# Kernel tuning notes

Hardware: AMD Instinct MI355X
Metric: run time of the kernel (lower is better)

Reference implementation:

```python
import jax, jax.numpy as jnp
import numpy as np


def setup_inputs() -> dict:
    key = jax.random.key(0)
    k1, k2, k3, k4, k5 = jax.random.split(key, 5)
    B, S, E, T = 64, 2048, 256, 100
    h = jax.random.normal(k1, (B, S, E), dtype=jnp.float32)
    theta = jax.random.uniform(k2, (B, T), dtype=jnp.float32)
    w = jax.random.normal(k3, (E, T), dtype=jnp.float32) * 0.05
    v = jax.random.normal(k4, (E, 1), dtype=jnp.float32) * 0.05
    u = jax.random.normal(k5, (E, E), dtype=jnp.float32) * 0.05
    return {"h": h, "theta": theta, "w": w, "v": v, "u": u}


def reference(h, theta, w, v, u):
    # h: [B,S,E], theta: [B,T], w: [E,T], v: [E,1], u: [E,E]
    theta_w = theta @ w.T                      # [B,E]
    h_u = jnp.einsum('bse,ef->bsf', h, u)      # [B,S,E]
    g = jnp.tanh(theta_w[:, None, :] + h_u) @ v  # [B,S,1]
    weight = jax.nn.softmax(g[..., 0], axis=-1)  # [B,S]
    vec = jnp.einsum('bs,bse->be', weight, h)    # [B,E]
    return vec
```

## Files before the change

kernel.cpp:

```cpp
#include <hip/hip_runtime.h>
#include <hip/hip_bf16.h>
#include <math.h>


#define E_DIM 256
#define GM 32
#define NC 8

typedef __bf16 bf16x8 __attribute__((ext_vector_type(8)));
typedef float  f32x4  __attribute__((ext_vector_type(4)));

__device__ __forceinline__ unsigned short f2bf(float x) {
    return __builtin_bit_cast(unsigned short, (__bf16)x);
}

__device__ __forceinline__ float fast_tanh(float x) {
    const float e = __expf(2.0f * x);
    const float r = __builtin_amdgcn_rcpf(e + 1.0f);
    return fmaf(-2.0f, r, 1.0f);
}

__device__ __forceinline__ unsigned sswz(unsigned slot, unsigned row) {
    return (slot & 48u) | ((slot & 15u) ^ (row & 15u));
}

__global__ __launch_bounds__(256) void k_prep(const float* __restrict__ u,
                                              const float* __restrict__ theta,
                                              const float* __restrict__ w,
                                              unsigned short* __restrict__ u_t,
                                              float* __restrict__ tw,
                                              int T) {
    if (blockIdx.x < 16) {
        __shared__ float tl[256 * 17];
        const int f0 = blockIdx.x * 16;
        const int tid = threadIdx.x;
        const int cl = tid & 15;
        const int rw = tid >> 4;
#pragma unroll
        for (int it = 0; it < 16; ++it) {
            const int e = it * 16 + rw;
            tl[e * 17 + cl] = u[(size_t)e * E_DIM + f0 + cl];
        }
        __syncthreads();
        unsigned short outv[16];
#pragma unroll
        for (int j = 0; j < 16; ++j)
            outv[j] = f2bf(tl[(cl * 16 + j) * 17 + rw]);
        *reinterpret_cast<uint4*>(u_t + (size_t)(f0 + rw) * E_DIM + cl * 16) =
            *reinterpret_cast<const uint4*>(outv);
        *reinterpret_cast<uint4*>(u_t + (size_t)(f0 + rw) * E_DIM + cl * 16 + 8) =
            *reinterpret_cast<const uint4*>(outv + 8);
    } else {
        __shared__ float th[128];
        const int b = blockIdx.x - 16;
        const int e = threadIdx.x;
        if (threadIdx.x < T) th[threadIdx.x] = theta[b * T + threadIdx.x];
        __syncthreads();
        float acc = 0.f;
        for (int t = 0; t < T; ++t) acc = fmaf(th[t], w[e * T + t], acc);
        tw[b * E_DIM + e] = acc;
    }
}

__global__
__attribute__((amdgpu_flat_work_group_size(256, 256), amdgpu_waves_per_eu(2, 2)))
void k_fused(const float* __restrict__ h,
             const unsigned short* __restrict__ u_t,
             const float* __restrict__ tw_,
             const float* __restrict__ v,
             float* __restrict__ partial,
             float* __restrict__ pd,
             int S, int SC) {
    __shared__ float Abuf[2][GM * E_DIM];
    __shared__ float red[4][GM];
    __shared__ float pacc[4][E_DIM];
    __shared__ float dred[4];

    const int b   = blockIdx.y;
    const int c0  = blockIdx.x * NC;
    const int tid = threadIdx.x;
    const int w   = tid >> 6;
    const int l   = tid & 63;
    const int lg  = l >> 4;
    const int lc  = l & 15;
    const int f0w = w * 64;

#define STAGE(buf, ch)                                                           \
    {                                                                            \
        const char* hb_ = (const char*)(h + ((size_t)b * S + (size_t)(ch) * GM) * E_DIM); \
        _Pragma("unroll")                                                        \
        for (int r = 0; r < 8; ++r) {                                            \
            const int row = r * 4 + w;                                           \
            const unsigned ss = sswz((unsigned)l, (unsigned)row);                \
            __builtin_amdgcn_global_load_lds(                                    \
                (const __attribute__((address_space(1))) void*)(hb_ + (size_t)row * 1024 + ss * 16), \
                (__attribute__((address_space(3))) void*)((char*)Abuf[buf] + r * 4096 + w * 1024), \
                16, 0, 0);                                                       \
        }                                                                        \
    }

    STAGE(0, c0);

    bf16x8 ub[8][4];
#pragma unroll
    for (int kt = 0; kt < 8; ++kt)
#pragma unroll
        for (int n = 0; n < 4; ++n)
            ub[kt][n] = *reinterpret_cast<const bf16x8*>(
                u_t + (size_t)(f0w + n * 16 + lc) * E_DIM + kt * 32 + lg * 8);

    float tw_f[4], v_f[4];
#pragma unroll
    for (int n = 0; n < 4; ++n) {
        const int f = f0w + n * 16 + lc;
        tw_f[n] = tw_[b * E_DIM + f];
        v_f[n]  = v[f];
    }

    f32x4 numa = (f32x4){0.f, 0.f, 0.f, 0.f};
    float den = 0.f;

    for (int c = 0; c < NC; ++c) {
        const int cur = c & 1;

        if (c + 1 < NC) {
            STAGE(cur ^ 1, c0 + c + 1);
            asm volatile("s_waitcnt vmcnt(8)" ::: "memory");
        } else {
            asm volatile("s_waitcnt vmcnt(0)" ::: "memory");
        }
        __builtin_amdgcn_s_barrier();
        __builtin_amdgcn_sched_barrier(0);

        const char* A = (const char*)Abuf[cur];
        f32x4 acc[2][4];
#pragma unroll
        for (int m = 0; m < 2; ++m)
#pragma unroll
            for (int n = 0; n < 4; ++n)
                acc[m][n] = (f32x4){0.f, 0.f, 0.f, 0.f};

#pragma unroll
        for (int kt = 0; kt < 8; ++kt) {
            bf16x8 af[2];
#pragma unroll
            for (int m = 0; m < 2; ++m) {
                const unsigned row = (unsigned)(m * 16 + lc);
                const unsigned s0 = sswz((unsigned)(kt * 8 + lg * 2), row);
                const unsigned s1 = sswz((unsigned)(kt * 8 + lg * 2 + 1), row);
                const f32x4 fa0 = *reinterpret_cast<const f32x4*>(A + row * 1024 + s0 * 16);
                const f32x4 fa1 = *reinterpret_cast<const f32x4*>(A + row * 1024 + s1 * 16);
#pragma unroll
                for (int j = 0; j < 4; ++j) {
                    af[m][j]     = (__bf16)fa0[j];
                    af[m][4 + j] = (__bf16)fa1[j];
                }
            }
#pragma unroll
            for (int n = 0; n < 4; ++n) {
                acc[0][n] = __builtin_amdgcn_mfma_f32_16x16x32_bf16(af[0], ub[kt][n], acc[0][n], 0, 0, 0);
                acc[1][n] = __builtin_amdgcn_mfma_f32_16x16x32_bf16(af[1], ub[kt][n], acc[1][n], 0, 0, 0);
            }
        }

        float rs[2][4] = {};
#pragma unroll
        for (int n = 0; n < 4; ++n)
#pragma unroll
            for (int m = 0; m < 2; ++m)
#pragma unroll
                for (int i = 0; i < 4; ++i)
                    rs[m][i] += fast_tanh(acc[m][n][i] + tw_f[n]) * v_f[n];

#pragma unroll
        for (int off = 1; off < 16; off <<= 1)
#pragma unroll
            for (int m = 0; m < 2; ++m)
#pragma unroll
                for (int i = 0; i < 4; ++i)
                    rs[m][i] += __shfl_xor(rs[m][i], off, 64);

        if (lc == 0) {
#pragma unroll
            for (int m = 0; m < 2; ++m)
#pragma unroll
                for (int i = 0; i < 4; ++i)
                    red[w][m * 16 + lg * 4 + i] = rs[m][i];
        }
        asm volatile("s_waitcnt lgkmcnt(0)" ::: "memory");
        __builtin_amdgcn_s_barrier();
        __builtin_amdgcn_sched_barrier(0);

#pragma unroll
        for (int j = 0; j < 8; ++j) {
            const unsigned row = (unsigned)(j * 4 + w);
            const float g = red[0][row] + red[1][row] + red[2][row] + red[3][row];
            const float ex = __expf(g);
            den += ex;
            const unsigned ss = sswz((unsigned)l, row);
            const f32x4 hv = *reinterpret_cast<const f32x4*>(A + row * 1024 + ss * 16);
            numa[0] = fmaf(ex, hv[0], numa[0]);
            numa[1] = fmaf(ex, hv[1], numa[1]);
            numa[2] = fmaf(ex, hv[2], numa[2]);
            numa[3] = fmaf(ex, hv[3], numa[3]);
        }
    }

    *reinterpret_cast<f32x4*>(&pacc[w][l * 4]) = numa;
    if (l == 0) dred[w] = den;
    __syncthreads();

    const int nb = SC / NC;
    partial[((size_t)b * nb + blockIdx.x) * E_DIM + tid] =
        pacc[0][tid] + pacc[1][tid] + pacc[2][tid] + pacc[3][tid];
    if (tid == 0)
        pd[(size_t)b * nb + blockIdx.x] = dred[0] + dred[1] + dred[2] + dred[3];
#undef STAGE
}

__global__ __launch_bounds__(256) void k_combine(const float* __restrict__ partial,
                                                 const float* __restrict__ pd,
                                                 float* __restrict__ out,
                                                 int NB) {
    const int b = blockIdx.x, t = threadIdx.x;
    float den = 0.f;
    for (int k = 0; k < NB; ++k) den += pd[(size_t)b * NB + k];
    float num = 0.f;
    for (int k = 0; k < NB; ++k)
        num += partial[((size_t)b * NB + k) * E_DIM + t];
    out[(size_t)b * E_DIM + t] = num / den;
}

extern "C" void kernel_launch(void* const* d_in, const int* in_sizes, int n_in,
                              void* d_out, int out_size, void* d_ws, size_t ws_size,
                              hipStream_t stream) {
    const float* h     = (const float*)d_in[0];
    const float* theta = (const float*)d_in[1];
    const float* w     = (const float*)d_in[2];
    const float* v     = (const float*)d_in[3];
    const float* u     = (const float*)d_in[4];
    float* out = (float*)d_out;

    const int E = in_sizes[3];
    const int T = in_sizes[2] / E;
    const int B = in_sizes[1] / T;
    const int S = in_sizes[0] / (B * E);
    const int SC = S / GM;
    const int NB = SC / NC;

    float* tw = (float*)d_ws;
    unsigned short* u_t = (unsigned short*)(tw + (size_t)B * E);
    float* partial = (float*)(u_t + (size_t)E * E);
    float* pd = partial + (size_t)B * NB * E;

    k_prep<<<dim3(16 + B), dim3(256), 0, stream>>>(u, theta, w, u_t, tw, T);
    k_fused<<<dim3(NB, B), dim3(256), 0, stream>>>(h, u_t, tw, v, partial, pd, S, SC);
    k_combine<<<dim3(B), dim3(256), 0, stream>>>(partial, pd, out, NB);
}
```

Before: 57.72 us.

## Defer softmax-weighted sum to next iteration to drop one barrier per chunk

The exp-weighted accumulation of the h rows for chunk c now runs at the start of iteration c+1, reading the score partials from a double-buffered `red` array. This removes the second workgroup barrier and the LDS wait inside each chunk iteration, leaving one barrier per chunk. In exchange, the prefetch of the next chunk into the shared buffer is issued only after that deferred sum finishes, and each iteration begins with a full vmcnt(0) wait. That shortens the window in which global loads overlap compute.

After: 59.09 us. 1.02x slower.

```diff
diff --git a/kernel.cpp b/kernel.cpp
--- a/kernel.cpp
+++ b/kernel.cpp
@@ -72,7 +72,7 @@
              float* __restrict__ pd,
              int S, int SC) {
     __shared__ float Abuf[2][GM * E_DIM];
-    __shared__ float red[4][GM];
+    __shared__ float red[2][4][GM];
     __shared__ float pacc[4][E_DIM];
     __shared__ float dred[4];
 
@@ -99,6 +99,24 @@
         }                                                                        \
     }
 
+#define WSUM(rbuf, Ap)                                                           \
+    {                                                                            \
+        _Pragma("unroll")                                                        \
+        for (int j = 0; j < 8; ++j) {                                            \
+            const unsigned row = (unsigned)(j * 4 + w);                          \
+            const float g = red[rbuf][0][row] + red[rbuf][1][row]                \
+                          + red[rbuf][2][row] + red[rbuf][3][row];               \
+            const float ex = __expf(g);                                          \
+            den += ex;                                                           \
+            const unsigned ss = sswz((unsigned)l, row);                          \
+            const f32x4 hv = *reinterpret_cast<const f32x4*>((Ap) + row * 1024 + ss * 16); \
+            numa[0] = fmaf(ex, hv[0], numa[0]);                                  \
+            numa[1] = fmaf(ex, hv[1], numa[1]);                                  \
+            numa[2] = fmaf(ex, hv[2], numa[2]);                                  \
+            numa[3] = fmaf(ex, hv[3], numa[3]);                                  \
+        }                                                                        \
+    }
+
     STAGE(0, c0);
 
     bf16x8 ub[8][4];
@@ -123,13 +141,17 @@
     for (int c = 0; c < NC; ++c) {
         const int cur = c & 1;
 
-        if (c + 1 < NC) {
-            STAGE(cur ^ 1, c0 + c + 1);
-            asm volatile("s_waitcnt vmcnt(8)" ::: "memory");
-        } else {
-            asm volatile("s_waitcnt vmcnt(0)" ::: "memory");
-        }
+        asm volatile("s_waitcnt vmcnt(0) lgkmcnt(0)" ::: "memory");
         __builtin_amdgcn_s_barrier();
+        __builtin_amdgcn_sched_barrier(0);
+
+        if (c >= 1) {
+            const char* Ap = (const char*)Abuf[cur ^ 1];
+            WSUM((c - 1) & 1, Ap);
+        }
+        __builtin_amdgcn_sched_barrier(0);
+
+        if (c + 1 < NC) STAGE(cur ^ 1, c0 + c + 1);
         __builtin_amdgcn_sched_barrier(0);
 
         const char* A = (const char*)Abuf[cur];
@@ -185,25 +207,15 @@
             for (int m = 0; m < 2; ++m)
 #pragma unroll
                 for (int i = 0; i < 4; ++i)
-                    red[w][m * 16 + lg * 4 + i] = rs[m][i];
-        }
-        asm volatile("s_waitcnt lgkmcnt(0)" ::: "memory");
-        __builtin_amdgcn_s_barrier();
-        __builtin_amdgcn_sched_barrier(0);
-
-#pragma unroll
-        for (int j = 0; j < 8; ++j) {
-            const unsigned row = (unsigned)(j * 4 + w);
-            const float g = red[0][row] + red[1][row] + red[2][row] + red[3][row];
-            const float ex = __expf(g);
-            den += ex;
-            const unsigned ss = sswz((unsigned)l, row);
-            const f32x4 hv = *reinterpret_cast<const f32x4*>(A + row * 1024 + ss * 16);
-            numa[0] = fmaf(ex, hv[0], numa[0]);
-            numa[1] = fmaf(ex, hv[1], numa[1]);
-            numa[2] = fmaf(ex, hv[2], numa[2]);
-            numa[3] = fmaf(ex, hv[3], numa[3]);
-        }
+                    red[cur][w][m * 16 + lg * 4 + i] = rs[m][i];
+        }
+    }
+
+    asm volatile("s_waitcnt lgkmcnt(0)" ::: "memory");
+    __builtin_amdgcn_s_barrier();
+    {
+        const char* Ap = (const char*)Abuf[(NC - 1) & 1];
+        WSUM((NC - 1) & 1, Ap);
     }
 
     *reinterpret_cast<f32x4*>(&pacc[w][l * 4]) = numa;
@@ -216,6 +228,7 @@
     if (tid == 0)
         pd[(size_t)b * nb + blockIdx.x] = dred[0] + dred[1] + dred[2] + dred[3];
 #undef STAGE
+#undef WSUM
 }
 
 __global__ __launch_bounds__(256) void k_combine(const float* __restrict__ partial,
```

## Fuse combine into main kernel via atomics and last-block ticket; compute theta·w per block

Applied to the files above, without the earlier changes.

Drops the separate combine kernel. Each block atomically adds its partial numerator and denominator into global accumulators, and the last block per batch (found with a ticket counter) writes the normalized output. The theta·w projection moves into the fused kernel, where each block recomputes it into shared memory, and the prep kernel now only zero-initializes the accumulators. This removes one launch and a partial-buffer round trip, at the cost of redundant theta·w work per block, atomic traffic, and non-deterministic float summation order.

After: 128.1 us. 122% more time.

```diff
diff --git a/kernel.cpp b/kernel.cpp
--- a/kernel.cpp
+++ b/kernel.cpp
@@ -6,6 +6,7 @@
 #define E_DIM 256
 #define GM 32
 #define NC 8
+#define NB 8
 
 typedef __bf16 bf16x8 __attribute__((ext_vector_type(8)));
 typedef float  f32x4  __attribute__((ext_vector_type(4)));
@@ -25,11 +26,10 @@
 }
 
 __global__ __launch_bounds__(256) void k_prep(const float* __restrict__ u,
-                                              const float* __restrict__ theta,
-                                              const float* __restrict__ w,
                                               unsigned short* __restrict__ u_t,
-                                              float* __restrict__ tw,
-                                              int T) {
+                                              float* __restrict__ num_acc,
+                                              float* __restrict__ den_acc,
+                                              int* __restrict__ ticket) {
     if (blockIdx.x < 16) {
         __shared__ float tl[256 * 17];
         const int f0 = blockIdx.x * 16;
@@ -51,14 +51,12 @@
         *reinterpret_cast<uint4*>(u_t + (size_t)(f0 + rw) * E_DIM + cl * 16 + 8) =
             *reinterpret_cast<const uint4*>(outv + 8);
     } else {
-        __shared__ float th[128];
         const int b = blockIdx.x - 16;
-        const int e = threadIdx.x;
-        if (threadIdx.x < T) th[threadIdx.x] = theta[b * T + threadIdx.x];
-        __syncthreads();
-        float acc = 0.f;
-        for (int t = 0; t < T; ++t) acc = fmaf(th[t], w[e * T + t], acc);
-        tw[b * E_DIM + e] = acc;
+        num_acc[(size_t)b * E_DIM + threadIdx.x] = 0.f;
+        if (threadIdx.x == 0) {
+            den_acc[b] = 0.f;
+            ticket[b] = 0;
+        }
     }
 }
 
@@ -66,15 +64,20 @@
 __attribute__((amdgpu_flat_work_group_size(256, 256), amdgpu_waves_per_eu(2, 2)))
 void k_fused(const float* __restrict__ h,
              const unsigned short* __restrict__ u_t,
-             const float* __restrict__ tw_,
+             const float* __restrict__ theta,
+             const float* __restrict__ wm,
              const float* __restrict__ v,
-             float* __restrict__ partial,
-             float* __restrict__ pd,
-             int S, int SC) {
+             float* __restrict__ num_acc,
+             float* __restrict__ den_acc,
+             int* __restrict__ ticket,
+             float* __restrict__ out,
+             int S, int SC, int T) {
     __shared__ float Abuf[2][GM * E_DIM];
     __shared__ float red[4][GM];
     __shared__ float pacc[4][E_DIM];
+    __shared__ float twl[E_DIM];
     __shared__ float dred[4];
+    __shared__ int lastFlag;
 
     const int b   = blockIdx.y;
     const int c0  = blockIdx.x * NC;
@@ -109,11 +112,20 @@
             ub[kt][n] = *reinterpret_cast<const bf16x8*>(
                 u_t + (size_t)(f0w + n * 16 + lc) * E_DIM + kt * 32 + lg * 8);
 
+    {
+        float acc = 0.f;
+        const float* thr = theta + (size_t)b * T;
+        const float* wr  = wm + (size_t)tid * T;
+        for (int t = 0; t < T; ++t) acc = fmaf(thr[t], wr[t], acc);
+        twl[tid] = acc;
+    }
+    __syncthreads();
+
     float tw_f[4], v_f[4];
 #pragma unroll
     for (int n = 0; n < 4; ++n) {
         const int f = f0w + n * 16 + lc;
-        tw_f[n] = tw_[b * E_DIM + f];
+        tw_f[n] = twl[f];
         v_f[n]  = v[f];
     }
 
@@ -210,25 +222,28 @@
     if (l == 0) dred[w] = den;
     __syncthreads();
 
-    const int nb = SC / NC;
-    partial[((size_t)b * nb + blockIdx.x) * E_DIM + tid] =
-        pacc[0][tid] + pacc[1][tid] + pacc[2][tid] + pacc[3][tid];
+    const float mysum = pacc[0][tid] + pacc[1][tid] + pacc[2][tid] + pacc[3][tid];
+    atomicAdd(&num_acc[(size_t)b * E_DIM + tid], mysum);
     if (tid == 0)
-        pd[(size_t)b * nb + blockIdx.x] = dred[0] + dred[1] + dred[2] + dred[3];
+        atomicAdd(&den_acc[b], dred[0] + dred[1] + dred[2] + dred[3]);
+    __threadfence();
+
+    if (tid == 0) {
+        const int old = atomicAdd(&ticket[b], 1);
+        lastFlag = (old == NB - 1);
+    }
+    __syncthreads();
+
+    if (lastFlag) {
+        __threadfence();
+        const float nsum = atomicAdd(&num_acc[(size_t)b * E_DIM + tid], 0.f);
+        float dsum;
+        if (tid == 0) dred[0] = atomicAdd(&den_acc[b], 0.f);
+        __syncthreads();
+        dsum = dred[0];
+        out[(size_t)b * E_DIM + tid] = nsum / dsum;
+    }
 #undef STAGE
-}
-
-__global__ __launch_bounds__(256) void k_combine(const float* __restrict__ partial,
-                                                 const float* __restrict__ pd,
-                                                 float* __restrict__ out,
-                                                 int NB) {
-    const int b = blockIdx.x, t = threadIdx.x;
-    float den = 0.f;
-    for (int k = 0; k < NB; ++k) den += pd[(size_t)b * NB + k];
-    float num = 0.f;
-    for (int k = 0; k < NB; ++k)
-        num += partial[((size_t)b * NB + k) * E_DIM + t];
-    out[(size_t)b * E_DIM + t] = num / den;
 }
 
 extern "C" void kernel_launch(void* const* d_in, const int* in_sizes, int n_in,
@@ -246,14 +261,13 @@
     const int B = in_sizes[1] / T;
     const int S = in_sizes[0] / (B * E);
     const int SC = S / GM;
-    const int NB = SC / NC;
-
-    float* tw = (float*)d_ws;
-    unsigned short* u_t = (unsigned short*)(tw + (size_t)B * E);
-    float* partial = (float*)(u_t + (size_t)E * E);
-    float* pd = partial + (size_t)B * NB * E;
-
-    k_prep<<<dim3(16 + B), dim3(256), 0, stream>>>(u, theta, w, u_t, tw, T);
-    k_fused<<<dim3(NB, B), dim3(256), 0, stream>>>(h, u_t, tw, v, partial, pd, S, SC);
-    k_combine<<<dim3(B), dim3(256), 0, stream>>>(partial, pd, out, NB);
-}
+
+    unsigned short* u_t = (unsigned short*)d_ws;
+    float* num_acc = (float*)(u_t + (size_t)E * E);
+    float* den_acc = num_acc + (size_t)B * E;
+    int*   ticket  = (int*)(den_acc + B);
+
+    k_prep<<<dim3(16 + B), dim3(256), 0, stream>>>(u, u_t, num_acc, den_acc, ticket);
+    k_fused<<<dim3(NB, B), dim3(256), 0, stream>>>(h, u_t, theta, w, v,
+                                                   num_acc, den_acc, ticket, out, S, SC, T);
+}
```
